# Kernel optimization log

Hardware: AMD Instinct MI355X
Metric: run time of the kernel (lower is better)

## Reference

```python
import jax, jax.numpy as jnp
import numpy as np

N = 100_000   # nodes
E = 1_600_000 # edges
F = 128       # num_features
H = 128       # hidden
L = 3         # num_conv_layers
G = 512       # graphs in batch
BN_EPS = 1e-5


def _xavier(key, shape):
    fan_in, fan_out = shape[-1], shape[-2]
    scale = jnp.sqrt(2.0 / (fan_in + fan_out))
    return jax.random.normal(key, shape, dtype=jnp.float32) * scale


def setup_inputs() -> dict:
    key = jax.random.key(0)
    ks = jax.random.split(key, 10)
    x = jax.random.normal(ks[0], (N, F), dtype=jnp.float32)
    edge_index = jax.random.randint(ks[1], (2, E), 0, N, dtype=jnp.int32)
    batch = jnp.sort(jax.random.randint(ks[2], (N,), 0, G, dtype=jnp.int32))
    return {
        "x": x,
        "edge_index": edge_index,
        "batch": batch,
        "t1_w": _xavier(ks[3], (H, F)),
        "t1_b": jnp.zeros((H,), jnp.float32),
        "t2_w": _xavier(ks[4], (H, H)),
        "t2_b": jnp.zeros((H,), jnp.float32),
        "W1": _xavier(ks[5], (L, H, H)),
        "b1": jnp.zeros((L, H), jnp.float32),
        "gamma": jnp.ones((L, H), jnp.float32),
        "beta": jnp.zeros((L, H), jnp.float32),
        "W2": _xavier(ks[6], (L, H, H)),
        "b2": jnp.zeros((L, H), jnp.float32),
    }


def reference(x, edge_index, batch, t1_w, t1_b, t2_w, t2_b, W1, b1, gamma, beta, W2, b2):
    src, dst = edge_index[0], edge_index[1]
    # input transform (dropout is identity in eval mode)
    h = jax.nn.relu(x @ t1_w.T + t1_b)  # [N, H]
    # BN eval mode: running_mean=0, running_var=1 -> affine scale only
    bn_scale = gamma * jax.lax.rsqrt(jnp.float32(1.0 + BN_EPS))  # [L, H]
    for l in range(L):
        # GINConv with eps=0: (1+eps)*h_i + sum_{j->i} h_j
        agg = jax.ops.segment_sum(h[src], dst, num_segments=N)  # [N, H]
        z = h + agg
        z = z @ W1[l].T + b1[l]
        z = z * bn_scale[l] + beta[l]
        z = jax.nn.relu(z)
        h = z @ W2[l].T + b2[l]
    h = h @ t2_w.T + t2_b  # [N, H]
    graph_emb = jax.ops.segment_sum(h, batch, num_segments=G)  # [G, H]
    return graph_emb
```

## Files before the change

### kernel.cpp

```cpp
#include <hip/hip_runtime.h>
#include <hip/hip_bf16.h>

#define NNODES 100000
#define NEDGES 1600000
#define NR     100096
#define NGRAPH 512
#define NB     782
#define NBLK_BIN 128
#define EPB    12500

typedef __attribute__((ext_vector_type(8))) __bf16 bf16x8;
typedef __attribute__((ext_vector_type(4))) float f32x4;
typedef __attribute__((ext_vector_type(4))) unsigned int u32x4;
typedef __attribute__((ext_vector_type(2))) unsigned int u32x2;

__device__ __forceinline__ float b2f(unsigned int u16) {
    union { float f; unsigned int i; } v; v.i = (u16 & 0xffffu) << 16; return v.f;
}
__device__ __forceinline__ unsigned short f2b(float f) {
    union { float f; unsigned int i; } v; v.f = f;
    unsigned int u = (v.i + 0x7fffu + ((v.i >> 16) & 1u)) >> 16;
    return (unsigned short)u;
}

__global__ __launch_bounds__(256) void wconv(const float* __restrict__ t1w,
                                             const float* __restrict__ t2w,
                                             const float* __restrict__ W1,
                                             const float* __restrict__ W2,
                                             unsigned short* __restrict__ Wb) {
    int i = blockIdx.x * 256 + threadIdx.x;
    float4 v;
    if (i < 4096)       v = reinterpret_cast<const float4*>(t1w)[i];
    else if (i < 8192)  v = reinterpret_cast<const float4*>(t2w)[i - 4096];
    else if (i < 20480) v = reinterpret_cast<const float4*>(W1)[i - 8192];
    else                v = reinterpret_cast<const float4*>(W2)[i - 20480];
    u32x2 o;
    o.x = (unsigned int)f2b(v.x) | ((unsigned int)f2b(v.y) << 16);
    o.y = (unsigned int)f2b(v.z) | ((unsigned int)f2b(v.w) << 16);
    *reinterpret_cast<u32x2*>(Wb + (size_t)i * 4) = o;
}

__global__ __launch_bounds__(256) void hist_k(const int* __restrict__ dst,
                                              int* __restrict__ ghist) {
    __shared__ int lh[NB];
    int blk = blockIdx.x, tid = threadIdx.x;
    for (int i = tid; i < NB; i += 256) lh[i] = 0;
    __syncthreads();
    int s = blk * EPB;
    for (int i = s + tid; i < s + EPB; i += 256) atomicAdd(&lh[dst[i] >> 7], 1);
    __syncthreads();
    for (int b = tid; b < NB; b += 256) ghist[b * NBLK_BIN + blk] = lh[b];
}

__global__ __launch_bounds__(256) void scan_pairs(const int* __restrict__ ghist,
                                                  int* __restrict__ off,
                                                  int* __restrict__ tot) {
    int wid = threadIdx.x >> 6, lane = threadIdx.x & 63;
    int b = blockIdx.x * 4 + wid;
    if (b >= NB) return;
    int v0 = ghist[b * NBLK_BIN + lane * 2];
    int v1 = ghist[b * NBLK_BIN + lane * 2 + 1];
    int s = v0 + v1, incl = s;
    for (int o = 1; o < 64; o <<= 1) {
        int t = __shfl_up(incl, o);
        if (lane >= o) incl += t;
    }
    int excl = incl - s;
    off[b * NBLK_BIN + lane * 2] = excl;
    off[b * NBLK_BIN + lane * 2 + 1] = excl + v0;
    if (lane == 63) tot[b] = incl;
}

__global__ __launch_bounds__(1024) void boff_scan(const int* __restrict__ tot,
                                                  int* __restrict__ boff) {
    __shared__ int sm[1024];
    int t = threadIdx.x;
    int v = (t < NB) ? tot[t] : 0;
    sm[t] = v;
    __syncthreads();
    for (int o = 1; o < 1024; o <<= 1) {
        int u = (t >= o) ? sm[t - o] : 0;
        __syncthreads();
        sm[t] += u;
        __syncthreads();
    }
    if (t < NB) boff[t] = sm[t] - v;
    if (t == NB - 1) boff[NB] = sm[t];
}

__global__ __launch_bounds__(256) void scatter2(const int* __restrict__ src,
                                                const int* __restrict__ dst,
                                                const int* __restrict__ off,
                                                const int* __restrict__ boff,
                                                unsigned int* __restrict__ binned) {
    __shared__ int lbase[NB];
    __shared__ int lcnt[NB];
    int blk = blockIdx.x, tid = threadIdx.x;
    for (int b = tid; b < NB; b += 256) {
        lbase[b] = boff[b] + off[b * NBLK_BIN + blk];
        lcnt[b] = 0;
    }
    __syncthreads();
    int s0 = blk * EPB;
    for (int i = s0 + tid; i < s0 + EPB; i += 256) {
        int d = dst[i];
        int b = d >> 7;
        int r = atomicAdd(&lcnt[b], 1);
        binned[lbase[b] + r] = (unsigned int)src[i] | ((unsigned int)(d & 127) << 17);
    }
}

__global__ __launch_bounds__(256) void csr_build(const int* __restrict__ boff,
                                                 const unsigned int* __restrict__ binned,
                                                 int* __restrict__ rowptr,
                                                 int* __restrict__ csr) {
    __shared__ int lhist[128], lscan[128], lcnt[128];
    int b = blockIdx.x, tid = threadIdx.x;
    int s = boff[b], e = boff[b + 1];
    if (tid < 128) { lhist[tid] = 0; lcnt[tid] = 0; }
    __syncthreads();
    for (int i = s + tid; i < e; i += 256)
        atomicAdd(&lhist[(binned[i] >> 17) & 127], 1);
    __syncthreads();
    if (tid < 128) lscan[tid] = lhist[tid];
    __syncthreads();
    for (int o = 1; o < 128; o <<= 1) {
        int v = (tid < 128 && tid >= o) ? lscan[tid - o] : 0;
        __syncthreads();
        if (tid < 128) lscan[tid] += v;
        __syncthreads();
    }
    if (tid < 128) {
        int n = b * 128 + tid;
        if (n <= NNODES) rowptr[n] = s + lscan[tid] - lhist[tid];
    }
    __syncthreads();
    for (int i = s + tid; i < e; i += 256) {
        unsigned int v = binned[i];
        int dl = (v >> 17) & 127;
        int r = atomicAdd(&lcnt[dl], 1);
        csr[s + lscan[dl] - lhist[dl] + r] = (int)(v & 0x1FFFFu);
    }
}

__global__ __launch_bounds__(512) void layer_fused(const unsigned short* __restrict__ hPrev,
                                                   const int* __restrict__ rowptr,
                                                   const int* __restrict__ csr,
                                                   const unsigned short* __restrict__ W1b,
                                                   const unsigned short* __restrict__ W2b,
                                                   const float* __restrict__ b1,
                                                   const float* __restrict__ gamma,
                                                   const float* __restrict__ beta,
                                                   const float* __restrict__ b2,
                                                   unsigned short* __restrict__ hNext) {
    __shared__ unsigned short lsZ[128 * 128];
    __shared__ unsigned short lsB[128 * 128];
    const int tid = threadIdx.x;
    const int w = tid >> 6;
    const int lane = tid & 63;
    const int nodeBase = blockIdx.x * 128;
    const int g  = lane >> 4;
    const int fl = lane & 15;

#pragma unroll
    for (int it = 0; it < 4; ++it) {
        int idx = it * 512 + tid;
        int row = idx >> 4, u = idx & 15;
        uint4 v = *reinterpret_cast<const uint4*>(W1b + (size_t)row * 128 + u * 8);
        *reinterpret_cast<uint4*>((char*)lsB + row * 256 + ((u * 16) ^ ((row & 7) << 4))) = v;
    }

    for (int nl = 0; nl < 16; ++nl) {
        const int lr = w * 16 + nl;
        const int node = nodeBase + lr;
        float a0 = 0.f, a1 = 0.f, a2 = 0.f, a3 = 0.f, a4 = 0.f, a5 = 0.f, a6 = 0.f, a7 = 0.f;
        int s = 0, e = 0;
        if (node < NNODES) { s = rowptr[node]; e = rowptr[node + 1]; }
        int i = s + g;
        for (; i + 12 < e; i += 16) {
            int j0 = csr[i];
            int j1 = csr[i + 4];
            int j2 = csr[i + 8];
            int j3 = csr[i + 12];
            u32x4 v0 = *reinterpret_cast<const u32x4*>(hPrev + (size_t)j0 * 128 + fl * 8);
            u32x4 v1 = *reinterpret_cast<const u32x4*>(hPrev + (size_t)j1 * 128 + fl * 8);
            u32x4 v2 = *reinterpret_cast<const u32x4*>(hPrev + (size_t)j2 * 128 + fl * 8);
            u32x4 v3 = *reinterpret_cast<const u32x4*>(hPrev + (size_t)j3 * 128 + fl * 8);
            a0 += b2f(v0.x); a1 += b2f(v0.x >> 16);
            a2 += b2f(v0.y); a3 += b2f(v0.y >> 16);
            a4 += b2f(v0.z); a5 += b2f(v0.z >> 16);
            a6 += b2f(v0.w); a7 += b2f(v0.w >> 16);
            a0 += b2f(v1.x); a1 += b2f(v1.x >> 16);
            a2 += b2f(v1.y); a3 += b2f(v1.y >> 16);
            a4 += b2f(v1.z); a5 += b2f(v1.z >> 16);
            a6 += b2f(v1.w); a7 += b2f(v1.w >> 16);
            a0 += b2f(v2.x); a1 += b2f(v2.x >> 16);
            a2 += b2f(v2.y); a3 += b2f(v2.y >> 16);
            a4 += b2f(v2.z); a5 += b2f(v2.z >> 16);
            a6 += b2f(v2.w); a7 += b2f(v2.w >> 16);
            a0 += b2f(v3.x); a1 += b2f(v3.x >> 16);
            a2 += b2f(v3.y); a3 += b2f(v3.y >> 16);
            a4 += b2f(v3.z); a5 += b2f(v3.z >> 16);
            a6 += b2f(v3.w); a7 += b2f(v3.w >> 16);
        }
        for (; i < e; i += 4) {
            int j0 = csr[i];
            u32x4 v0 = *reinterpret_cast<const u32x4*>(hPrev + (size_t)j0 * 128 + fl * 8);
            a0 += b2f(v0.x); a1 += b2f(v0.x >> 16);
            a2 += b2f(v0.y); a3 += b2f(v0.y >> 16);
            a4 += b2f(v0.z); a5 += b2f(v0.z >> 16);
            a6 += b2f(v0.w); a7 += b2f(v0.w >> 16);
        }
        a0 += __shfl_xor(a0, 16); a1 += __shfl_xor(a1, 16);
        a2 += __shfl_xor(a2, 16); a3 += __shfl_xor(a3, 16);
        a4 += __shfl_xor(a4, 16); a5 += __shfl_xor(a5, 16);
        a6 += __shfl_xor(a6, 16); a7 += __shfl_xor(a7, 16);
        a0 += __shfl_xor(a0, 32); a1 += __shfl_xor(a1, 32);
        a2 += __shfl_xor(a2, 32); a3 += __shfl_xor(a3, 32);
        a4 += __shfl_xor(a4, 32); a5 += __shfl_xor(a5, 32);
        a6 += __shfl_xor(a6, 32); a7 += __shfl_xor(a7, 32);
        if (g == 0) {
            u32x4 sv = *reinterpret_cast<const u32x4*>(hPrev + (size_t)node * 128 + fl * 8);
            a0 += b2f(sv.x); a1 += b2f(sv.x >> 16);
            a2 += b2f(sv.y); a3 += b2f(sv.y >> 16);
            a4 += b2f(sv.z); a5 += b2f(sv.z >> 16);
            a6 += b2f(sv.w); a7 += b2f(sv.w >> 16);
            u32x4 o;
            o.x = (unsigned int)f2b(a0) | ((unsigned int)f2b(a1) << 16);
            o.y = (unsigned int)f2b(a2) | ((unsigned int)f2b(a3) << 16);
            o.z = (unsigned int)f2b(a4) | ((unsigned int)f2b(a5) << 16);
            o.w = (unsigned int)f2b(a6) | ((unsigned int)f2b(a7) << 16);
            *reinterpret_cast<u32x4*>((char*)lsZ + lr * 256 + ((fl * 16) ^ ((lr & 7) << 4))) = o;
        }
    }
    __syncthreads();

    const int wr = w >> 1, wc = w & 1;
    f32x4 acc[2][4];
    f32x4 zv = {0.f, 0.f, 0.f, 0.f};
#pragma unroll
    for (int m = 0; m < 2; ++m)
#pragma unroll
        for (int n = 0; n < 4; ++n) acc[m][n] = zv;
#pragma unroll
    for (int ks = 0; ks < 4; ++ks) {
        int kbb = ks * 64 + ((lane >> 4) << 4);
        bf16x8 af[2], bfr[4];
#pragma unroll
        for (int m = 0; m < 2; ++m) {
            int ar = wr * 32 + m * 16 + (lane & 15);
            af[m] = *reinterpret_cast<const bf16x8*>((char*)lsZ + ar * 256 + (kbb ^ ((ar & 7) << 4)));
        }
#pragma unroll
        for (int n = 0; n < 4; ++n) {
            int bc = wc * 64 + n * 16 + (lane & 15);
            bfr[n] = *reinterpret_cast<const bf16x8*>((char*)lsB + bc * 256 + (kbb ^ ((bc & 7) << 4)));
        }
#pragma unroll
        for (int m = 0; m < 2; ++m)
#pragma unroll
            for (int n = 0; n < 4; ++n)
                acc[m][n] = __builtin_amdgcn_mfma_f32_16x16x32_bf16(af[m], bfr[n], acc[m][n], 0, 0, 0);
    }
    __syncthreads();

#pragma unroll
    for (int n = 0; n < 4; ++n) {
        int col = wc * 64 + n * 16 + (lane & 15);
        float bb = b1[col];
        float sc = gamma[col] * rsqrtf(1.0f + 1e-5f);
        float bt = beta[col];
#pragma unroll
        for (int m = 0; m < 2; ++m) {
            int r0 = wr * 32 + m * 16 + ((lane >> 4) << 2);
#pragma unroll
            for (int r = 0; r < 4; ++r) {
                float v = (acc[m][n][r] + bb) * sc + bt;
                v = fmaxf(v, 0.f);
                int row = r0 + r;
                *(unsigned short*)((char*)lsZ + row * 256 + ((2 * col) ^ ((row & 7) << 4))) = f2b(v);
            }
        }
    }
#pragma unroll
    for (int it = 0; it < 4; ++it) {
        int idx = it * 512 + tid;
        int row = idx >> 4, u = idx & 15;
        uint4 v = *reinterpret_cast<const uint4*>(W2b + (size_t)row * 128 + u * 8);
        *reinterpret_cast<uint4*>((char*)lsB + row * 256 + ((u * 16) ^ ((row & 7) << 4))) = v;
    }
    __syncthreads();

    f32x4 acc2[2][4];
#pragma unroll
    for (int m = 0; m < 2; ++m)
#pragma unroll
        for (int n = 0; n < 4; ++n) acc2[m][n] = zv;
#pragma unroll
    for (int ks = 0; ks < 4; ++ks) {
        int kbb = ks * 64 + ((lane >> 4) << 4);
        bf16x8 af[2], bfr[4];
#pragma unroll
        for (int m = 0; m < 2; ++m) {
            int ar = wr * 32 + m * 16 + (lane & 15);
            af[m] = *reinterpret_cast<const bf16x8*>((char*)lsZ + ar * 256 + (kbb ^ ((ar & 7) << 4)));
        }
#pragma unroll
        for (int n = 0; n < 4; ++n) {
            int bc = wc * 64 + n * 16 + (lane & 15);
            bfr[n] = *reinterpret_cast<const bf16x8*>((char*)lsB + bc * 256 + (kbb ^ ((bc & 7) << 4)));
        }
#pragma unroll
        for (int m = 0; m < 2; ++m)
#pragma unroll
            for (int n = 0; n < 4; ++n)
                acc2[m][n] = __builtin_amdgcn_mfma_f32_16x16x32_bf16(af[m], bfr[n], acc2[m][n], 0, 0, 0);
    }

#pragma unroll
    for (int n = 0; n < 4; ++n) {
        int col = wc * 64 + n * 16 + (lane & 15);
        float bb = b2[col];
#pragma unroll
        for (int m = 0; m < 2; ++m) {
            int r0 = nodeBase + wr * 32 + m * 16 + ((lane >> 4) << 2);
#pragma unroll
            for (int r = 0; r < 4; ++r)
                hNext[(size_t)(r0 + r) * 128 + col] = f2b(acc2[m][n][r] + bb);
        }
    }
}

template <int SRC_F32, int MODE>
__global__ __launch_bounds__(256) void gemm128(const void* __restrict__ Asrc, int src_rows,
                                               const unsigned short* __restrict__ Wb,
                                               const float* __restrict__ bias,
                                               unsigned short* __restrict__ Out) {
    __shared__ unsigned short lsA[128 * 128];
    __shared__ unsigned short lsB[128 * 128];
    const int tid = threadIdx.x;
    const int blockRow = blockIdx.x * 128;

    for (int it = 0; it < 8; ++it) {
        int idx = it * 256 + tid;
        int row = idx >> 4;
        int u = idx & 15;
        uint4 v = *reinterpret_cast<const uint4*>(Wb + (size_t)row * 128 + u * 8);
        int boffb = row * 256 + ((u * 16) ^ ((row & 7) << 4));
        *reinterpret_cast<uint4*>((char*)lsB + boffb) = v;
    }
    if (SRC_F32) {
        const float* A = (const float*)Asrc;
        for (int it = 0; it < 16; ++it) {
            int fidx = it * 256 + tid;
            int row = fidx >> 5;
            int c4 = (fidx & 31) * 4;
            int gr = blockRow + row; if (gr > src_rows - 1) gr = src_rows - 1;
            float4 v = *reinterpret_cast<const float4*>(A + (size_t)gr * 128 + c4);
            int boffb = row * 256 + ((c4 * 2) ^ ((row & 7) << 4));
            unsigned short* p = (unsigned short*)((char*)lsA + boffb);
            p[0] = f2b(v.x); p[1] = f2b(v.y); p[2] = f2b(v.z); p[3] = f2b(v.w);
        }
    } else {
        const unsigned short* A = (const unsigned short*)Asrc;
        for (int it = 0; it < 8; ++it) {
            int idx = it * 256 + tid;
            int row = idx >> 4;
            int u = idx & 15;
            int gr = blockRow + row;
            uint4 v = *reinterpret_cast<const uint4*>(A + (size_t)gr * 128 + u * 8);
            int boffb = row * 256 + ((u * 16) ^ ((row & 7) << 4));
            *reinterpret_cast<uint4*>((char*)lsA + boffb) = v;
        }
    }
    __syncthreads();

    const int lane = tid & 63;
    const int w = tid >> 6;
    const int wr = w >> 1, wc = w & 1;

    f32x4 acc[4][4];
    f32x4 zv = {0.f, 0.f, 0.f, 0.f};
#pragma unroll
    for (int m = 0; m < 4; ++m)
#pragma unroll
        for (int n = 0; n < 4; ++n) acc[m][n] = zv;

#pragma unroll
    for (int ks = 0; ks < 4; ++ks) {
        int kbb = ks * 64 + ((lane >> 4) << 4);
        bf16x8 af[4], bfr[4];
#pragma unroll
        for (int m = 0; m < 4; ++m) {
            int ar = wr * 64 + m * 16 + (lane & 15);
            af[m] = *reinterpret_cast<const bf16x8*>((char*)lsA + ar * 256 + (kbb ^ ((ar & 7) << 4)));
        }
#pragma unroll
        for (int n = 0; n < 4; ++n) {
            int bc = wc * 64 + n * 16 + (lane & 15);
            bfr[n] = *reinterpret_cast<const bf16x8*>((char*)lsB + bc * 256 + (kbb ^ ((bc & 7) << 4)));
        }
#pragma unroll
        for (int m = 0; m < 4; ++m)
#pragma unroll
            for (int n = 0; n < 4; ++n)
                acc[m][n] = __builtin_amdgcn_mfma_f32_16x16x32_bf16(af[m], bfr[n], acc[m][n], 0, 0, 0);
    }

#pragma unroll
    for (int n = 0; n < 4; ++n) {
        int col = wc * 64 + n * 16 + (lane & 15);
        float bb = bias[col];
#pragma unroll
        for (int m = 0; m < 4; ++m) {
            int r0 = blockRow + wr * 64 + m * 16 + ((lane >> 4) << 2);
#pragma unroll
            for (int r = 0; r < 4; ++r) {
                float v = acc[m][n][r] + bb;
                if (MODE >= 1) v = fmaxf(v, 0.f);
                Out[(size_t)(r0 + r) * 128 + col] = f2b(v);
            }
        }
    }
}

__global__ __launch_bounds__(128) void segsum(const unsigned short* __restrict__ hf,
                                              const int* __restrict__ batch,
                                              float* __restrict__ out) {
    int g = blockIdx.x, f = threadIdx.x;
    int lo = 0, hi = NNODES;
    while (lo < hi) { int mid = (lo + hi) >> 1; if (batch[mid] < g) lo = mid + 1; else hi = mid; }
    int s = lo;
    lo = 0; hi = NNODES;
    while (lo < hi) { int mid = (lo + hi) >> 1; if (batch[mid] < g + 1) lo = mid + 1; else hi = mid; }
    int e = lo;
    float acc0 = 0.f, acc1 = 0.f, acc2 = 0.f, acc3 = 0.f;
    int n = s;
    for (; n + 3 < e; n += 4) {
        acc0 += b2f(hf[(size_t)n * 128 + f]);
        acc1 += b2f(hf[(size_t)(n + 1) * 128 + f]);
        acc2 += b2f(hf[(size_t)(n + 2) * 128 + f]);
        acc3 += b2f(hf[(size_t)(n + 3) * 128 + f]);
    }
    for (; n < e; ++n) acc0 += b2f(hf[(size_t)n * 128 + f]);
    out[(size_t)g * 128 + f] = (acc0 + acc1) + (acc2 + acc3);
}

extern "C" void kernel_launch(void* const* d_in, const int* in_sizes, int n_in,
                              void* d_out, int out_size, void* d_ws, size_t ws_size,
                              hipStream_t stream) {
    const float* x     = (const float*)d_in[0];
    const int*   ei    = (const int*)d_in[1];
    const int*   batch = (const int*)d_in[2];
    const float* t1w   = (const float*)d_in[3];
    const float* t1b   = (const float*)d_in[4];
    const float* t2w   = (const float*)d_in[5];
    const float* t2b   = (const float*)d_in[6];
    const float* W1    = (const float*)d_in[7];
    const float* b1    = (const float*)d_in[8];
    const float* gamma = (const float*)d_in[9];
    const float* beta  = (const float*)d_in[10];
    const float* W2    = (const float*)d_in[11];
    const float* b2    = (const float*)d_in[12];
    float* out = (float*)d_out;

    char* ws = (char*)d_ws;
    size_t off_b = 0;
    auto alloc = [&](size_t bytes) -> void* {
        off_b = (off_b + 511) & ~size_t(511);
        void* p = ws + off_b;
        off_b += bytes;
        return p;
    };
    unsigned short* hbA = (unsigned short*)alloc((size_t)NR * 128 * 2);
    unsigned short* hbB = (unsigned short*)alloc((size_t)NR * 128 * 2);
    unsigned short* Wb  = (unsigned short*)alloc((size_t)131072 * 2);
    int* rowptr         = (int*)alloc((size_t)(NNODES + 2) * 4);
    int* ghist          = (int*)alloc((size_t)NB * NBLK_BIN * 4);
    int* off            = (int*)alloc((size_t)NB * NBLK_BIN * 4);
    int* tot            = (int*)alloc((size_t)NB * 4);
    int* boff           = (int*)alloc((size_t)(NB + 1) * 4);
    unsigned int* binned = (unsigned int*)alloc((size_t)NEDGES * 4);
    int* csr            = (int*)alloc((size_t)NEDGES * 4);

    const int* esrc = ei;
    const int* edst = ei + NEDGES;

    wconv<<<128, 256, 0, stream>>>(t1w, t2w, W1, W2, Wb);

    hist_k<<<NBLK_BIN, 256, 0, stream>>>(edst, ghist);
    scan_pairs<<<(NB + 3) / 4, 256, 0, stream>>>(ghist, off, tot);
    boff_scan<<<1, 1024, 0, stream>>>(tot, boff);
    scatter2<<<NBLK_BIN, 256, 0, stream>>>(esrc, edst, off, boff, binned);
    csr_build<<<NB, 256, 0, stream>>>(boff, binned, rowptr, csr);

    gemm128<1, 1><<<NR / 128, 256, 0, stream>>>(x, NNODES, Wb, t1b, hbA);

    const unsigned short* hin = hbA;
    unsigned short* hout = hbB;
    for (int l = 0; l < 3; ++l) {
        layer_fused<<<NB, 512, 0, stream>>>(hin, rowptr, csr,
                                            Wb + 32768 + (size_t)l * 16384,
                                            Wb + 81920 + (size_t)l * 16384,
                                            b1 + l * 128, gamma + l * 128, beta + l * 128,
                                            b2 + l * 128, hout);
        unsigned short* t = (unsigned short*)hin; hin = hout; hout = t;
    }
    gemm128<0, 0><<<NR / 128, 256, 0, stream>>>(hin, NR, Wb + 16384, t2b, hout);
    segsum<<<NGRAPH, 128, 0, stream>>>(hout, batch, out);
}
```

Baseline: 557.7 us.

## Split fused GIN layer into separate aggregation and MLP kernels

Splits the fused per-layer kernel into a gather-aggregation kernel with one wavefront per node over many small blocks, followed by a separate MLP GEMM kernel that reads the aggregated rows from global memory. The aim is better latency hiding and load balance for the irregular gather, which was limited by large 512-thread blocks using 64KB of LDS each. The cost is an extra round trip of the aggregated features through global memory and an extra launch per layer. Buffers are reused so the MLP writes back into the input buffer.

```diff
diff --git a/kernel.cpp b/kernel.cpp
--- a/kernel.cpp
+++ b/kernel.cpp
@@ -143,95 +143,107 @@
     }
 }
 
-__global__ __launch_bounds__(512) void layer_fused(const unsigned short* __restrict__ hPrev,
-                                                   const int* __restrict__ rowptr,
-                                                   const int* __restrict__ csr,
-                                                   const unsigned short* __restrict__ W1b,
-                                                   const unsigned short* __restrict__ W2b,
-                                                   const float* __restrict__ b1,
-                                                   const float* __restrict__ gamma,
-                                                   const float* __restrict__ beta,
-                                                   const float* __restrict__ b2,
-                                                   unsigned short* __restrict__ hNext) {
+__global__ __launch_bounds__(256) void agg_node4(const unsigned short* __restrict__ hb,
+                                                 const int* __restrict__ rowptr,
+                                                 const int* __restrict__ csr,
+                                                 unsigned short* __restrict__ zb) {
+    int wid = threadIdx.x >> 6, lane = threadIdx.x & 63;
+    int node = blockIdx.x * 4 + wid;
+    if (node >= NNODES) return;
+    const int g  = lane >> 4;
+    const int fl = lane & 15;
+
+    float a0 = 0.f, a1 = 0.f, a2 = 0.f, a3 = 0.f, a4 = 0.f, a5 = 0.f, a6 = 0.f, a7 = 0.f;
+    const int s = rowptr[node], e = rowptr[node + 1];
+
+    int i = s + g;
+    for (; i + 12 < e; i += 16) {
+        int j0 = csr[i];
+        int j1 = csr[i + 4];
+        int j2 = csr[i + 8];
+        int j3 = csr[i + 12];
+        u32x4 v0 = *reinterpret_cast<const u32x4*>(hb + (size_t)j0 * 128 + fl * 8);
+        u32x4 v1 = *reinterpret_cast<const u32x4*>(hb + (size_t)j1 * 128 + fl * 8);
+        u32x4 v2 = *reinterpret_cast<const u32x4*>(hb + (size_t)j2 * 128 + fl * 8);
+        u32x4 v3 = *reinterpret_cast<const u32x4*>(hb + (size_t)j3 * 128 + fl * 8);
+        a0 += b2f(v0.x); a1 += b2f(v0.x >> 16);
+        a2 += b2f(v0.y); a3 += b2f(v0.y >> 16);
+        a4 += b2f(v0.z); a5 += b2f(v0.z >> 16);
+        a6 += b2f(v0.w); a7 += b2f(v0.w >> 16);
+        a0 += b2f(v1.x); a1 += b2f(v1.x >> 16);
+        a2 += b2f(v1.y); a3 += b2f(v1.y >> 16);
+        a4 += b2f(v1.z); a5 += b2f(v1.z >> 16);
+        a6 += b2f(v1.w); a7 += b2f(v1.w >> 16);
+        a0 += b2f(v2.x); a1 += b2f(v2.x >> 16);
+        a2 += b2f(v2.y); a3 += b2f(v2.y >> 16);
+        a4 += b2f(v2.z); a5 += b2f(v2.z >> 16);
+        a6 += b2f(v2.w); a7 += b2f(v2.w >> 16);
+        a0 += b2f(v3.x); a1 += b2f(v3.x >> 16);
+        a2 += b2f(v3.y); a3 += b2f(v3.y >> 16);
+        a4 += b2f(v3.z); a5 += b2f(v3.z >> 16);
+        a6 += b2f(v3.w); a7 += b2f(v3.w >> 16);
+    }
+    for (; i < e; i += 4) {
+        int j0 = csr[i];
+        u32x4 v0 = *reinterpret_cast<const u32x4*>(hb + (size_t)j0 * 128 + fl * 8);
+        a0 += b2f(v0.x); a1 += b2f(v0.x >> 16);
+        a2 += b2f(v0.y); a3 += b2f(v0.y >> 16);
+        a4 += b2f(v0.z); a5 += b2f(v0.z >> 16);
+        a6 += b2f(v0.w); a7 += b2f(v0.w >> 16);
+    }
+
+    a0 += __shfl_xor(a0, 16); a1 += __shfl_xor(a1, 16);
+    a2 += __shfl_xor(a2, 16); a3 += __shfl_xor(a3, 16);
+    a4 += __shfl_xor(a4, 16); a5 += __shfl_xor(a5, 16);
+    a6 += __shfl_xor(a6, 16); a7 += __shfl_xor(a7, 16);
+    a0 += __shfl_xor(a0, 32); a1 += __shfl_xor(a1, 32);
+    a2 += __shfl_xor(a2, 32); a3 += __shfl_xor(a3, 32);
+    a4 += __shfl_xor(a4, 32); a5 += __shfl_xor(a5, 32);
+    a6 += __shfl_xor(a6, 32); a7 += __shfl_xor(a7, 32);
+
+    if (g == 0) {
+        u32x4 sv = *reinterpret_cast<const u32x4*>(hb + (size_t)node * 128 + fl * 8);
+        a0 += b2f(sv.x); a1 += b2f(sv.x >> 16);
+        a2 += b2f(sv.y); a3 += b2f(sv.y >> 16);
+        a4 += b2f(sv.z); a5 += b2f(sv.z >> 16);
+        a6 += b2f(sv.w); a7 += b2f(sv.w >> 16);
+        u32x4 o;
+        o.x = (unsigned int)f2b(a0) | ((unsigned int)f2b(a1) << 16);
+        o.y = (unsigned int)f2b(a2) | ((unsigned int)f2b(a3) << 16);
+        o.z = (unsigned int)f2b(a4) | ((unsigned int)f2b(a5) << 16);
+        o.w = (unsigned int)f2b(a6) | ((unsigned int)f2b(a7) << 16);
+        *reinterpret_cast<u32x4*>(zb + (size_t)node * 128 + fl * 8) = o;
+    }
+}
+
+__global__ __launch_bounds__(512) void mlp128(const unsigned short* __restrict__ zb,
+                                              const unsigned short* __restrict__ W1b,
+                                              const unsigned short* __restrict__ W2b,
+                                              const float* __restrict__ b1,
+                                              const float* __restrict__ gamma,
+                                              const float* __restrict__ beta,
+                                              const float* __restrict__ b2,
+                                              unsigned short* __restrict__ hNext) {
     __shared__ unsigned short lsZ[128 * 128];
     __shared__ unsigned short lsB[128 * 128];
     const int tid = threadIdx.x;
     const int w = tid >> 6;
     const int lane = tid & 63;
-    const int nodeBase = blockIdx.x * 128;
-    const int g  = lane >> 4;
-    const int fl = lane & 15;
-
+    const int blockRow = blockIdx.x * 128;
+
+#pragma unroll
+    for (int it = 0; it < 4; ++it) {
+        int idx = it * 512 + tid;
+        int row = idx >> 4, u = idx & 15;
+        uint4 v = *reinterpret_cast<const uint4*>(zb + (size_t)(blockRow + row) * 128 + u * 8);
+        *reinterpret_cast<uint4*>((char*)lsZ + row * 256 + ((u * 16) ^ ((row & 7) << 4))) = v;
+    }
 #pragma unroll
     for (int it = 0; it < 4; ++it) {
         int idx = it * 512 + tid;
         int row = idx >> 4, u = idx & 15;
         uint4 v = *reinterpret_cast<const uint4*>(W1b + (size_t)row * 128 + u * 8);
         *reinterpret_cast<uint4*>((char*)lsB + row * 256 + ((u * 16) ^ ((row & 7) << 4))) = v;
-    }
-
-    for (int nl = 0; nl < 16; ++nl) {
-        const int lr = w * 16 + nl;
-        const int node = nodeBase + lr;
-        float a0 = 0.f, a1 = 0.f, a2 = 0.f, a3 = 0.f, a4 = 0.f, a5 = 0.f, a6 = 0.f, a7 = 0.f;
-        int s = 0, e = 0;
-        if (node < NNODES) { s = rowptr[node]; e = rowptr[node + 1]; }
-        int i = s + g;
-        for (; i + 12 < e; i += 16) {
-            int j0 = csr[i];
-            int j1 = csr[i + 4];
-            int j2 = csr[i + 8];
-            int j3 = csr[i + 12];
-            u32x4 v0 = *reinterpret_cast<const u32x4*>(hPrev + (size_t)j0 * 128 + fl * 8);
-            u32x4 v1 = *reinterpret_cast<const u32x4*>(hPrev + (size_t)j1 * 128 + fl * 8);
-            u32x4 v2 = *reinterpret_cast<const u32x4*>(hPrev + (size_t)j2 * 128 + fl * 8);
-            u32x4 v3 = *reinterpret_cast<const u32x4*>(hPrev + (size_t)j3 * 128 + fl * 8);
-            a0 += b2f(v0.x); a1 += b2f(v0.x >> 16);
-            a2 += b2f(v0.y); a3 += b2f(v0.y >> 16);
-            a4 += b2f(v0.z); a5 += b2f(v0.z >> 16);
-            a6 += b2f(v0.w); a7 += b2f(v0.w >> 16);
-            a0 += b2f(v1.x); a1 += b2f(v1.x >> 16);
-            a2 += b2f(v1.y); a3 += b2f(v1.y >> 16);
-            a4 += b2f(v1.z); a5 += b2f(v1.z >> 16);
-            a6 += b2f(v1.w); a7 += b2f(v1.w >> 16);
-            a0 += b2f(v2.x); a1 += b2f(v2.x >> 16);
-            a2 += b2f(v2.y); a3 += b2f(v2.y >> 16);
-            a4 += b2f(v2.z); a5 += b2f(v2.z >> 16);
-            a6 += b2f(v2.w); a7 += b2f(v2.w >> 16);
-            a0 += b2f(v3.x); a1 += b2f(v3.x >> 16);
-            a2 += b2f(v3.y); a3 += b2f(v3.y >> 16);
-            a4 += b2f(v3.z); a5 += b2f(v3.z >> 16);
-            a6 += b2f(v3.w); a7 += b2f(v3.w >> 16);
-        }
-        for (; i < e; i += 4) {
-            int j0 = csr[i];
-            u32x4 v0 = *reinterpret_cast<const u32x4*>(hPrev + (size_t)j0 * 128 + fl * 8);
-            a0 += b2f(v0.x); a1 += b2f(v0.x >> 16);
-            a2 += b2f(v0.y); a3 += b2f(v0.y >> 16);
-            a4 += b2f(v0.z); a5 += b2f(v0.z >> 16);
-            a6 += b2f(v0.w); a7 += b2f(v0.w >> 16);
-        }
-        a0 += __shfl_xor(a0, 16); a1 += __shfl_xor(a1, 16);
-        a2 += __shfl_xor(a2, 16); a3 += __shfl_xor(a3, 16);
-        a4 += __shfl_xor(a4, 16); a5 += __shfl_xor(a5, 16);
-        a6 += __shfl_xor(a6, 16); a7 += __shfl_xor(a7, 16);
-        a0 += __shfl_xor(a0, 32); a1 += __shfl_xor(a1, 32);
-        a2 += __shfl_xor(a2, 32); a3 += __shfl_xor(a3, 32);
-        a4 += __shfl_xor(a4, 32); a5 += __shfl_xor(a5, 32);
-        a6 += __shfl_xor(a6, 32); a7 += __shfl_xor(a7, 32);
-        if (g == 0) {
-            u32x4 sv = *reinterpret_cast<const u32x4*>(hPrev + (size_t)node * 128 + fl * 8);
-            a0 += b2f(sv.x); a1 += b2f(sv.x >> 16);
-            a2 += b2f(sv.y); a3 += b2f(sv.y >> 16);
-            a4 += b2f(sv.z); a5 += b2f(sv.z >> 16);
-            a6 += b2f(sv.w); a7 += b2f(sv.w >> 16);
-            u32x4 o;
-            o.x = (unsigned int)f2b(a0) | ((unsigned int)f2b(a1) << 16);
-            o.y = (unsigned int)f2b(a2) | ((unsigned int)f2b(a3) << 16);
-            o.z = (unsigned int)f2b(a4) | ((unsigned int)f2b(a5) << 16);
-            o.w = (unsigned int)f2b(a6) | ((unsigned int)f2b(a7) << 16);
-            *reinterpret_cast<u32x4*>((char*)lsZ + lr * 256 + ((fl * 16) ^ ((lr & 7) << 4))) = o;
-        }
     }
     __syncthreads();
 
@@ -323,7 +335,7 @@
         float bb = b2[col];
 #pragma unroll
         for (int m = 0; m < 2; ++m) {
-            int r0 = nodeBase + wr * 32 + m * 16 + ((lane >> 4) << 2);
+            int r0 = blockRow + wr * 32 + m * 16 + ((lane >> 4) << 2);
 #pragma unroll
             for (int r = 0; r < 4; ++r)
                 hNext[(size_t)(r0 + r) * 128 + col] = f2b(acc2[m][n][r] + bb);
@@ -473,7 +485,7 @@
         return p;
     };
     unsigned short* hbA = (unsigned short*)alloc((size_t)NR * 128 * 2);
-    unsigned short* hbB = (unsigned short*)alloc((size_t)NR * 128 * 2);
+    unsigned short* zb  = (unsigned short*)alloc((size_t)NR * 128 * 2);
     unsigned short* Wb  = (unsigned short*)alloc((size_t)131072 * 2);
     int* rowptr         = (int*)alloc((size_t)(NNODES + 2) * 4);
     int* ghist          = (int*)alloc((size_t)NB * NBLK_BIN * 4);
@@ -496,16 +508,14 @@
 
     gemm128<1, 1><<<NR / 128, 256, 0, stream>>>(x, NNODES, Wb, t1b, hbA);
 
-    const unsigned short* hin = hbA;
-    unsigned short* hout = hbB;
     for (int l = 0; l < 3; ++l) {
-        layer_fused<<<NB, 512, 0, stream>>>(hin, rowptr, csr,
-                                            Wb + 32768 + (size_t)l * 16384,
-                                            Wb + 81920 + (size_t)l * 16384,
-                                            b1 + l * 128, gamma + l * 128, beta + l * 128,
-                                            b2 + l * 128, hout);
-        unsigned short* t = (unsigned short*)hin; hin = hout; hout = t;
-    }
-    gemm128<0, 0><<<NR / 128, 256, 0, stream>>>(hin, NR, Wb + 16384, t2b, hout);
-    segsum<<<NGRAPH, 128, 0, stream>>>(hout, batch, out);
-}
+        agg_node4<<<25000, 256, 0, stream>>>(hbA, rowptr, csr, zb);
+        mlp128<<<NB, 512, 0, stream>>>(zb,
+                                       Wb + 32768 + (size_t)l * 16384,
+                                       Wb + 81920 + (size_t)l * 16384,
+                                       b1 + l * 128, gamma + l * 128, beta + l * 128,
+                                       b2 + l * 128, hbA);
+    }
+    gemm128<0, 0><<<NR / 128, 256, 0, stream>>>(hbA, NR, Wb + 16384, t2b, zb);
+    segsum<<<NGRAPH, 128, 0, stream>>>(zb, batch, out);
+}
```

Measured after the change: 459.4 us. 17.6% less time.
